# Kernel tuning notes

Hardware: AMD Instinct MI355X
Metric: run time of the kernel (lower is better)

The kernel has to match this reference:

```python
import jax, jax.numpy as jnp
import numpy as np

DIM = 256; SEQ = 2048; WIN = 64; HEADS = 4; RANK = 32; LAYERS = 3; VOCAB = 32000
EPS = 1e-6

def _unit(v):
    # unit_normalize_values: project onto unit sphere along feature dim
    return v / jnp.maximum(jnp.linalg.norm(v, axis=-1, keepdims=True), EPS)

def _signed_softmax(s):
    # signed_softmax_state: sign(s) * softmax(|s|) over nodes
    return jnp.sign(s) * jax.nn.softmax(jnp.abs(s), axis=-1)

def setup_inputs() -> dict:
    key = jax.random.key(0)
    ks = jax.random.split(key, 10)
    d = DIM
    return {
        "input_ids": jax.random.randint(ks[0], (2, SEQ), 0, VOCAB, dtype=jnp.int32),
        "emb": 0.02 * jax.random.normal(ks[1], (VOCAB, d), jnp.float32),
        "pos_emb": 0.02 * jax.random.normal(ks[2], (SEQ, d), jnp.float32),
        "anchor_val": 0.02 * jax.random.normal(ks[3], (d,), jnp.float32),
        "anchor_state": jnp.zeros((), jnp.float32),
        "Ws": 0.02 * jax.random.normal(ks[4], (d,), jnp.float32),
        "bs": jnp.zeros((), jnp.float32),
        "U": 0.02 * jax.random.normal(ks[5], (LAYERS, d, HEADS, RANK), jnp.float32),
        "V": 0.02 * jax.random.normal(ks[6], (LAYERS, d, HEADS, RANK), jnp.float32),
        "W1": 0.02 * jax.random.normal(ks[7], (LAYERS, d, 2 * d), jnp.float32),
        "b1": jnp.zeros((LAYERS, 2 * d), jnp.float32),
        "W2": 0.02 * jax.random.normal(ks[8], (LAYERS, 2 * d, d), jnp.float32),
        "b2": jnp.zeros((LAYERS, d), jnp.float32),
    }

def _forward(emb, pos_emb, anchor_val, anchor_state, Ws, bs, U, V, W1, b1, W2, b2, input_ids):
    B, S = input_ids.shape
    tok = emb[input_ids] + pos_emb[None, :S]          # [B,S,D]
    state_src = tok                                    # state projected from pre-unit-norm values
    tok = _unit(tok)
    tstate = state_src @ Ws + bs                       # [B,S] scalar state per node
    val = jnp.concatenate([jnp.broadcast_to(_unit(anchor_val), (B, 1, DIM)), tok], axis=1)
    state = jnp.concatenate([jnp.broadcast_to(anchor_state, (B, 1)), tstate], axis=1)
    N = S + 1
    offs = jnp.arange(-WIN, WIN + 1)
    idx = jnp.arange(N)[:, None] + offs[None, :]       # [N,K]
    valid = (idx >= 0) & (idx < N)
    idxc = jnp.clip(idx, 0, N - 1)
    inv_sqrt_r = np.float32(1.0 / np.sqrt(RANK))
    for l in range(LAYERS):
        q = jnp.einsum('bnd,dhr->bnhr', val, U[l])
        k = jnp.einsum('bnd,dhr->bnhr', val, V[l])
        knb = k[:, idxc]                               # [B,N,K,H,R] window gather
        s = jnp.einsum('bnhr,bnkhr->bnkh', q, knb) * inv_sqrt_r
        s = s.max(axis=-1)                             # max head-aggregate [B,N,K]
        a = jnp.where(valid, jnp.abs(s), -jnp.inf)
        wgt = jnp.where(valid, jnp.sign(s) * jax.nn.softmax(a, axis=-1), 0.0)  # signed-abs-softmax edges
        dval = jnp.einsum('bnk,bnkd->bnd', wgt, val[:, idxc])
        dstate = jnp.sum(wgt * state[:, idxc], axis=-1)
        # apply_delta: residual + norm(identity) + unit-norm + touched-mask where
        updated = val + dval
        nv = _unit(updated)
        touched = jnp.max(jnp.abs(jax.lax.stop_gradient(dval)), axis=-1, keepdims=True) > 0
        val = jnp.where(touched, nv, updated)
        state = _signed_softmax(state + dstate)
        # residual feed-forward then re-unit-norm
        h = jax.nn.gelu(jnp.einsum('bnd,dh->bnh', val, W1[l]) + b1[l], approximate=False)
        val = _unit(val + jnp.einsum('bnh,hd->bnd', h, W2[l]) + b2[l])
    return state, val

def reference(input_ids, emb, pos_emb, anchor_val, anchor_state, Ws, bs, U, V, W1, b1, W2, b2):
    return _forward(emb, pos_emb, anchor_val, anchor_state, Ws, bs, U, V, W1, b1, W2, b2, input_ids)
```

## Files before the change

### kernel.cpp

```cpp
#include <hip/hip_runtime.h>
#include <hip/hip_bf16.h>
#include <math.h>

#define BB 2
#define SS 2048
#define NN 2049
#define MM (BB*NN)
#define DD 256
#define HR 128
#define NHEAD 4
#define WINW 64
#define DFF 512
#define EPSF 1e-6f
#define TB8 257

typedef __attribute__((ext_vector_type(8))) short bf16x8;
typedef __attribute__((ext_vector_type(4))) float f32x4;

__device__ __forceinline__ float wave_sum(float v) {
    v += __shfl_down(v, 32, 64); v += __shfl_down(v, 16, 64);
    v += __shfl_down(v, 8, 64);  v += __shfl_down(v, 4, 64);
    v += __shfl_down(v, 2, 64);  v += __shfl_down(v, 1, 64);
    return v;
}
__device__ __forceinline__ float wave_max(float v) {
    v = fmaxf(v, __shfl_down(v, 32, 64)); v = fmaxf(v, __shfl_down(v, 16, 64));
    v = fmaxf(v, __shfl_down(v, 8, 64));  v = fmaxf(v, __shfl_down(v, 4, 64));
    v = fmaxf(v, __shfl_down(v, 2, 64));  v = fmaxf(v, __shfl_down(v, 1, 64));
    return v;
}
__device__ __forceinline__ float block_sum(float v, float* red) {
    v = wave_sum(v);
    __syncthreads();
    if ((threadIdx.x & 63) == 0) red[threadIdx.x >> 6] = v;
    __syncthreads();
    return red[0] + red[1] + red[2] + red[3];
}
__device__ __forceinline__ float sgnf(float x) {
    return (x > 0.f) ? 1.f : ((x < 0.f) ? -1.f : 0.f);
}
__device__ __forceinline__ ushort f2b(float x) {
    __hip_bfloat16 h = __float2bfloat16(x);
    return *(ushort*)&h;
}
__device__ __forceinline__ float b2f(ushort u) {
    unsigned int v = ((unsigned int)u) << 16;
    return *(float*)&v;
}
__device__ __forceinline__ void split3(float x, ushort& h, ushort& m, ushort& l) {
    h = f2b(x);
    float r1 = x - b2f(h);
    m = f2b(r1);
    l = f2b(r1 - b2f(m));
}
__device__ __forceinline__ void pack_map(int e, int N, int& k, int& n) {
    int j = e & 7;
    int l = (e >> 3) & 63;
    int c = e >> 9;
    int ntiles = N >> 4;
    int kt = c / ntiles, nt = c - kt * ntiles;
    k = kt * 32 + ((l >> 4) << 3) + j;
    n = nt * 16 + (l & 15);
}
__device__ __forceinline__ void dma16(const ushort* g, ushort* lds) {
    __builtin_amdgcn_global_load_lds(
        (const __attribute__((address_space(1))) unsigned int*)g,
        (__attribute__((address_space(3))) unsigned int*)lds,
        16, 0, 0);
}

__global__ void packall_kernel(const float* __restrict__ W1, const float* __restrict__ W2,
                               const float* __restrict__ U,  const float* __restrict__ V,
                               ushort* __restrict__ W1ph, ushort* __restrict__ W1pl,
                               ushort* __restrict__ W2ph, ushort* __restrict__ W2pl,
                               ushort* __restrict__ U0, ushort* __restrict__ U1,
                               ushort* __restrict__ U2,
                               ushort* __restrict__ V0, ushort* __restrict__ V1,
                               ushort* __restrict__ V2) {
    int idx = blockIdx.x * 256 + threadIdx.x;
    int l = idx / 327680;
    int r = idx - l * 327680;
    if (l >= 3) return;
    int k, n;
    if (r < 131072) {
        int e = r;
        pack_map(e, 512, k, n);
        float s = W1[(size_t)l * 131072 + (size_t)k * 512 + n];
        ushort h = f2b(s);
        W1ph[(size_t)l * 131072 + e] = h;
        W1pl[(size_t)l * 131072 + e] = f2b(s - b2f(h));
    } else if (r < 262144) {
        int e = r - 131072;
        pack_map(e, 256, k, n);
        float s = W2[(size_t)l * 131072 + (size_t)k * 256 + n];
        ushort h = f2b(s);
        W2ph[(size_t)l * 131072 + e] = h;
        W2pl[(size_t)l * 131072 + e] = f2b(s - b2f(h));
    } else if (r < 294912) {
        int e = r - 262144;
        pack_map(e, 128, k, n);
        ushort h, m, lo;
        split3(U[(size_t)l * 32768 + (size_t)k * 128 + n], h, m, lo);
        U0[(size_t)l * 32768 + e] = h;
        U1[(size_t)l * 32768 + e] = m;
        U2[(size_t)l * 32768 + e] = lo;
    } else {
        int e = r - 294912;
        pack_map(e, 128, k, n);
        ushort h, m, lo;
        split3(V[(size_t)l * 32768 + (size_t)k * 128 + n], h, m, lo);
        V0[(size_t)l * 32768 + e] = h;
        V1[(size_t)l * 32768 + e] = m;
        V2[(size_t)l * 32768 + e] = lo;
    }
}

__global__ void embed_kernel(const int* __restrict__ ids,
                             const float* __restrict__ emb,
                             const float* __restrict__ pos,
                             const float* __restrict__ anchor_val,
                             const float* __restrict__ anchor_state,
                             const float* __restrict__ Ws,
                             const float* __restrict__ bs,
                             float* __restrict__ val,
                             ushort* __restrict__ v0, ushort* __restrict__ v1,
                             ushort* __restrict__ v2,
                             float* __restrict__ state) {
    __shared__ float red[4];
    int row = blockIdx.x;
    int t = threadIdx.x;
    int b = row / NN, n = row % NN;
    float e;
    if (n == 0) {
        e = anchor_val[t];
    } else {
        int id = ids[b * SS + (n - 1)];
        e = emb[(size_t)id * DD + t] + pos[(size_t)(n - 1) * DD + t];
    }
    float ss = block_sum(e * e, red);
    float ts = block_sum(e * Ws[t], red);
    float rn = 1.f / fmaxf(sqrtf(ss), EPSF);
    float o = e * rn;
    size_t oi = (size_t)row * DD + t;
    val[oi] = o;
    ushort h, m, lo;
    split3(o, h, m, lo);
    v0[oi] = h; v1[oi] = m; v2[oi] = lo;
    if (t == 0) state[row] = (n == 0) ? anchor_state[0] : (ts + bs[0]);
}

__global__ __launch_bounds__(256, 2)
void proj_kernel(const ushort* __restrict__ X0, const ushort* __restrict__ X1,
                 const ushort* __restrict__ X2,
                 const ushort* __restrict__ U0, const ushort* __restrict__ U1,
                 const ushort* __restrict__ U2,
                 const ushort* __restrict__ V0, const ushort* __restrict__ V1,
                 const ushort* __restrict__ V2,
                 ushort* __restrict__ q0, ushort* __restrict__ q1,
                 ushort* __restrict__ q2,
                 ushort* __restrict__ k0, ushort* __restrict__ k1,
                 ushort* __restrict__ k2) {
    __shared__ __align__(16) ushort stage[2][24 * 512];
    int t = threadIdx.x;
    int w = t >> 6, l = t & 63;
    int lm = l & 15, quad = l >> 4;
    int m0 = blockIdx.x * 16;
    bool isQ = (blockIdx.y == 0);
    const ushort* P0 = isQ ? U0 : V0;
    const ushort* P1 = isQ ? U1 : V1;
    const ushort* P2 = isQ ? U2 : V2;
    const ushort* P[3] = {P0, P1, P2};
    int row0 = m0 + lm; if (row0 > MM - 1) row0 = MM - 1;

    #pragma unroll
    for (int i = 0; i < 6; i++) {
        int c = w * 6 + i;
        int p = c >> 3, ntl = c & 7;
        dma16(P[p] + ((size_t)(0 * 8 + ntl) * 64 + l) * 8,
              &stage[0][c * 512 + l * 8]);
    }
    __syncthreads();

    f32x4 acc[2];
    acc[0] = (f32x4)(0.f); acc[1] = (f32x4)(0.f);
    for (int kt = 0; kt < 8; kt++) {
        int cur = kt & 1;
        if (kt < 7) {
            #pragma unroll
            for (int i = 0; i < 6; i++) {
                int c = w * 6 + i;
                int p = c >> 3, ntl = c & 7;
                dma16(P[p] + ((size_t)((kt + 1) * 8 + ntl) * 64 + l) * 8,
                      &stage[cur ^ 1][c * 512 + l * 8]);
            }
        }
        int ko = kt * 32 + quad * 8;
        bf16x8 a0 = *(const bf16x8*)(X0 + (size_t)row0 * DD + ko);
        bf16x8 a1 = *(const bf16x8*)(X1 + (size_t)row0 * DD + ko);
        bf16x8 a2 = *(const bf16x8*)(X2 + (size_t)row0 * DD + ko);
        #pragma unroll
        for (int jj = 0; jj < 2; jj++) {
            int ntl = w * 2 + jj;
            bf16x8 b0 = *(const bf16x8*)&stage[cur][(0 * 8 + ntl) * 512 + l * 8];
            bf16x8 b1 = *(const bf16x8*)&stage[cur][(1 * 8 + ntl) * 512 + l * 8];
            bf16x8 b2 = *(const bf16x8*)&stage[cur][(2 * 8 + ntl) * 512 + l * 8];
            acc[jj] = __builtin_amdgcn_mfma_f32_16x16x32_bf16(a0, b0, acc[jj], 0, 0, 0);
            acc[jj] = __builtin_amdgcn_mfma_f32_16x16x32_bf16(a0, b1, acc[jj], 0, 0, 0);
            acc[jj] = __builtin_amdgcn_mfma_f32_16x16x32_bf16(a1, b0, acc[jj], 0, 0, 0);
            acc[jj] = __builtin_amdgcn_mfma_f32_16x16x32_bf16(a1, b1, acc[jj], 0, 0, 0);
            acc[jj] = __builtin_amdgcn_mfma_f32_16x16x32_bf16(a0, b2, acc[jj], 0, 0, 0);
            acc[jj] = __builtin_amdgcn_mfma_f32_16x16x32_bf16(a2, b0, acc[jj], 0, 0, 0);
        }
        __syncthreads();
    }
    ushort* o0 = isQ ? q0 : k0;
    ushort* o1 = isQ ? q1 : k1;
    ushort* o2 = isQ ? q2 : k2;
    #pragma unroll
    for (int jj = 0; jj < 2; jj++) {
        int n = (w * 2 + jj) * 16 + lm;
        #pragma unroll
        for (int r = 0; r < 4; r++) {
            int tok = m0 + quad * 4 + r;
            if (tok < MM) {
                ushort h, m, lo;
                split3(acc[jj][r], h, m, lo);
                size_t oi = (size_t)tok * HR + n;
                o0[oi] = h; o1[oi] = m; o2[oi] = lo;
            }
        }
    }
}

__global__ __launch_bounds__(256, 2)
void attn_kernel(const float* __restrict__ val_in,
                 const float* __restrict__ state_in,
                 const ushort* __restrict__ q0, const ushort* __restrict__ q1,
                 const ushort* __restrict__ q2,
                 const ushort* __restrict__ k0, const ushort* __restrict__ k1,
                 const ushort* __restrict__ k2,
                 float* __restrict__ val_out,
                 ushort* __restrict__ vbH, ushort* __restrict__ vbM,
                 float* __restrict__ dstate_out) {
    __shared__ float sc4[NHEAD][8][148];
    __shared__ float wgt2[144][12];
    __shared__ float redS[8][4];
    __shared__ float redM[8][4];

    int b = blockIdx.x / TB8;
    int n0 = (blockIdx.x % TB8) * 8;
    int t = threadIdx.x;
    int w = t >> 6, l = t & 63;
    int lm = l & 15, quad = l >> 4;

    {
        int qrow = n0 + (lm & 7);
        if (qrow > NN - 1) qrow = NN - 1;
        size_t qa = ((size_t)(b * NN + qrow)) * HR + w * 32 + quad * 8;
        bf16x8 a0 = *(const bf16x8*)(q0 + qa);
        bf16x8 a1 = *(const bf16x8*)(q1 + qa);
        bf16x8 a2 = *(const bf16x8*)(q2 + qa);
        bf16x8 kf0[9], kf1[9], kf2[9];
        #pragma unroll
        for (int jt = 0; jt < 9; jt++) {
            int j = n0 - 64 + jt * 16 + lm;
            j = (j < 0) ? 0 : ((j > NN - 1) ? NN - 1 : j);
            size_t ka = ((size_t)(b * NN + j)) * HR + w * 32 + quad * 8;
            kf0[jt] = *(const bf16x8*)(k0 + ka);
            kf1[jt] = *(const bf16x8*)(k1 + ka);
            kf2[jt] = *(const bf16x8*)(k2 + ka);
        }
        #pragma unroll
        for (int jt = 0; jt < 9; jt++) {
            f32x4 acc = (f32x4)(0.f);
            acc = __builtin_amdgcn_mfma_f32_16x16x32_bf16(a0, kf0[jt], acc, 0, 0, 0);
            acc = __builtin_amdgcn_mfma_f32_16x16x32_bf16(a0, kf1[jt], acc, 0, 0, 0);
            acc = __builtin_amdgcn_mfma_f32_16x16x32_bf16(a1, kf0[jt], acc, 0, 0, 0);
            acc = __builtin_amdgcn_mfma_f32_16x16x32_bf16(a1, kf1[jt], acc, 0, 0, 0);
            acc = __builtin_amdgcn_mfma_f32_16x16x32_bf16(a0, kf2[jt], acc, 0, 0, 0);
            acc = __builtin_amdgcn_mfma_f32_16x16x32_bf16(a2, kf0[jt], acc, 0, 0, 0);
            if (quad < 2) {
                #pragma unroll
                for (int r = 0; r < 4; r++)
                    sc4[w][quad * 4 + r][jt * 16 + lm] = acc[r];
            }
        }
    }
    __syncthreads();

    {
        int m = t >> 5, p = t & 31;
        int n = n0 + m;
        bool tokv = (n < NN);
        float sv[5]; bool vv[5];
        float mx = -INFINITY;
        #pragma unroll
        for (int i = 0; i < 5; i++) {
            int tap = p + 32 * i;
            bool inb = (tap < 144);
            int tapc = inb ? tap : 0;
            int j = n0 - 64 + tapc;
            float s0 = sc4[0][m][tapc], s1 = sc4[1][m][tapc];
            float s2 = sc4[2][m][tapc], s3 = sc4[3][m][tapc];
            float s = fmaxf(fmaxf(s0, s1), fmaxf(s2, s3)) * 0.17677669529663687f;
            bool v = inb && tokv && (tap >= m) && (tap <= m + 128) && (j >= 0) && (j < NN);
            sv[i] = s; vv[i] = v;
            if (v) mx = fmaxf(mx, fabsf(s));
        }
        for (int off = 16; off > 0; off >>= 1) mx = fmaxf(mx, __shfl_xor(mx, off, 64));
        float ee[5];
        float sum = 0.f;
        #pragma unroll
        for (int i = 0; i < 5; i++) {
            ee[i] = vv[i] ? expf(fabsf(sv[i]) - mx) : 0.f;
            sum += ee[i];
        }
        for (int off = 16; off > 0; off >>= 1) sum += __shfl_xor(sum, off, 64);
        float inv = (sum > 0.f) ? 1.f / sum : 0.f;
        float ds = 0.f;
        #pragma unroll
        for (int i = 0; i < 5; i++) {
            int tap = p + 32 * i;
            if (tap < 144) {
                float wg = vv[i] ? sgnf(sv[i]) * ee[i] * inv : 0.f;
                wgt2[tap][m] = wg;
                if (vv[i]) ds += wg * state_in[b * NN + (n0 - 64 + tap)];
            }
        }
        for (int off = 16; off > 0; off >>= 1) ds += __shfl_xor(ds, off, 64);
        if (p == 0 && tokv) dstate_out[b * NN + n] = ds;
    }
    __syncthreads();

    {
        int d = (t >> 2) * 4;
        int tg = t & 3;
        int tok0 = tg * 2, tok1 = tg * 2 + 1;
        int jlo = (n0 >= 64) ? 0 : (64 - n0);
        int jhi = NN - 1 - n0 + 64; if (jhi > 135) jhi = 135;
        const float* vbase = val_in + ((size_t)(b * NN + n0 - 64)) * DD + d;
        f32x4 acc0 = (f32x4)(0.f), acc1 = (f32x4)(0.f);
        int jj = jlo;
        for (; jj + 3 <= jhi; jj += 4) {
            f32x4 v0 = *(const f32x4*)(vbase + (size_t)(jj + 0) * DD);
            f32x4 v1 = *(const f32x4*)(vbase + (size_t)(jj + 1) * DD);
            f32x4 v2 = *(const f32x4*)(vbase + (size_t)(jj + 2) * DD);
            f32x4 v3 = *(const f32x4*)(vbase + (size_t)(jj + 3) * DD);
            float wa0 = wgt2[jj + 0][tok0], wa1 = wgt2[jj + 0][tok1];
            float wb0 = wgt2[jj + 1][tok0], wb1 = wgt2[jj + 1][tok1];
            float wc0 = wgt2[jj + 2][tok0], wc1 = wgt2[jj + 2][tok1];
            float wd0 = wgt2[jj + 3][tok0], wd1 = wgt2[jj + 3][tok1];
            #pragma unroll
            for (int c = 0; c < 4; c++) {
                acc0[c] += v0[c] * wa0 + v1[c] * wb0 + v2[c] * wc0 + v3[c] * wd0;
                acc1[c] += v0[c] * wa1 + v1[c] * wb1 + v2[c] * wc1 + v3[c] * wd1;
            }
        }
        for (; jj <= jhi; jj++) {
            f32x4 v = *(const f32x4*)(vbase + (size_t)jj * DD);
            float w0 = wgt2[jj][tok0], w1 = wgt2[jj][tok1];
            #pragma unroll
            for (int c = 0; c < 4; c++) {
                acc0[c] += v[c] * w0;
                acc1[c] += v[c] * w1;
            }
        }
        f32x4 u[2]; f32x4 ac[2]; ac[0] = acc0; ac[1] = acc1;
        #pragma unroll
        for (int ti = 0; ti < 2; ti++) {
            int tok = tg * 2 + ti;
            int n = n0 + tok;
            f32x4 vold = (f32x4)(0.f);
            if (n < NN) vold = *(const f32x4*)(val_in + ((size_t)(b * NN + n)) * DD + d);
            u[ti] = vold + ac[ti];
            float s = u[ti][0]*u[ti][0] + u[ti][1]*u[ti][1] + u[ti][2]*u[ti][2] + u[ti][3]*u[ti][3];
            float mb = fmaxf(fmaxf(fabsf(ac[ti][0]), fabsf(ac[ti][1])),
                             fmaxf(fabsf(ac[ti][2]), fabsf(ac[ti][3])));
            for (int off = 4; off <= 32; off <<= 1) {
                s += __shfl_xor(s, off, 64);
                mb = fmaxf(mb, __shfl_xor(mb, off, 64));
            }
            if ((l >> 2) == 0) { redS[tok][w] = s; redM[tok][w] = mb; }
        }
        __syncthreads();
        #pragma unroll
        for (int ti = 0; ti < 2; ti++) {
            int tok = tg * 2 + ti;
            int n = n0 + tok;
            if (n < NN) {
                float ss = redS[tok][0] + redS[tok][1] + redS[tok][2] + redS[tok][3];
                float mab = fmaxf(fmaxf(redM[tok][0], redM[tok][1]),
                                  fmaxf(redM[tok][2], redM[tok][3]));
                float rn = 1.f / fmaxf(sqrtf(ss), EPSF);
                f32x4 o = u[ti];
                if (mab > 0.f) { o[0] *= rn; o[1] *= rn; o[2] *= rn; o[3] *= rn; }
                size_t oi = ((size_t)(b * NN + n)) * DD + d;
                *(f32x4*)(val_out + oi) = o;
                ushort4 hv, mv;
                {
                    ushort h0 = f2b(o[0]); hv.x = h0; mv.x = f2b(o[0] - b2f(h0));
                    ushort h1 = f2b(o[1]); hv.y = h1; mv.y = f2b(o[1] - b2f(h1));
                    ushort h2 = f2b(o[2]); hv.z = h2; mv.z = f2b(o[2] - b2f(h2));
                    ushort h3 = f2b(o[3]); hv.w = h3; mv.w = f2b(o[3] - b2f(h3));
                }
                *(ushort4*)(vbH + oi) = hv;
                *(ushort4*)(vbM + oi) = mv;
            }
        }
    }
}

__global__ __launch_bounds__(256, 2)
void ffn1_kernel(const ushort* __restrict__ XbH, const ushort* __restrict__ XbM,
                 const ushort* __restrict__ W1h, const ushort* __restrict__ W1l,
                 const float*  __restrict__ b1,
                 ushort* __restrict__ Hh, ushort* __restrict__ Hl,
                 const float* __restrict__ state_in, const float* __restrict__ dstate,
                 float* __restrict__ state_out) {
    __shared__ __align__(16) ushort stage[2][32 * 512];
    int t = threadIdx.x;

    if (blockIdx.x == 257) {
        float* red = (float*)&stage[0][0];
        int b = blockIdx.y;
        float lmax = -INFINITY;
        for (int n = t; n < NN; n += 256) {
            float x = state_in[b * NN + n] + dstate[b * NN + n];
            lmax = fmaxf(lmax, fabsf(x));
        }
        lmax = wave_max(lmax);
        if ((t & 63) == 0) red[t >> 6] = lmax;
        __syncthreads();
        float m = fmaxf(fmaxf(red[0], red[1]), fmaxf(red[2], red[3]));
        float lsum = 0.f;
        for (int n = t; n < NN; n += 256)
            lsum += expf(fabsf(state_in[b * NN + n] + dstate[b * NN + n]) - m);
        lsum = wave_sum(lsum);
        __syncthreads();
        if ((t & 63) == 0) red[4 + (t >> 6)] = lsum;
        __syncthreads();
        float inv = 1.f / (red[4] + red[5] + red[6] + red[7]);
        for (int n = t; n < NN; n += 256) {
            float x = state_in[b * NN + n] + dstate[b * NN + n];
            state_out[b * NN + n] = sgnf(x) * expf(fabsf(x) - m) * inv;
        }
        return;
    }

    int w = t >> 6, l = t & 63;
    int lm = l & 15, quad = l >> 4;
    int m0 = blockIdx.x * 16;
    int nh = blockIdx.y;
    int row0 = m0 + lm; if (row0 > MM - 1) row0 = MM - 1;

    #pragma unroll
    for (int i = 0; i < 8; i++) {
        int c = w * 8 + i;
        int p = c >> 4, ntl = c & 15;
        const ushort* src = (p ? W1l : W1h) + ((size_t)(0 * 32 + nh * 16 + ntl) * 64 + l) * 8;
        dma16(src, &stage[0][c * 512 + l * 8]);
    }
    __syncthreads();

    f32x4 acc[4];
    #pragma unroll
    for (int jj = 0; jj < 4; jj++) acc[jj] = (f32x4)(0.f);

    for (int kt = 0; kt < 8; kt++) {
        int cur = kt & 1;
        if (kt < 7) {
            #pragma unroll
            for (int i = 0; i < 8; i++) {
                int c = w * 8 + i;
                int p = c >> 4, ntl = c & 15;
                const ushort* src = (p ? W1l : W1h) +
                    ((size_t)((kt + 1) * 32 + nh * 16 + ntl) * 64 + l) * 8;
                dma16(src, &stage[cur ^ 1][c * 512 + l * 8]);
            }
        }
        int ko = kt * 32 + quad * 8;
        bf16x8 ah = *(const bf16x8*)(XbH + (size_t)row0 * DD + ko);
        bf16x8 am = *(const bf16x8*)(XbM + (size_t)row0 * DD + ko);
        #pragma unroll
        for (int jj = 0; jj < 4; jj++) {
            int ntl = w * 4 + jj;
            bf16x8 bh = *(const bf16x8*)&stage[cur][ntl * 512 + l * 8];
            bf16x8 bl = *(const bf16x8*)&stage[cur][(16 + ntl) * 512 + l * 8];
            acc[jj] = __builtin_amdgcn_mfma_f32_16x16x32_bf16(ah, bh, acc[jj], 0, 0, 0);
            acc[jj] = __builtin_amdgcn_mfma_f32_16x16x32_bf16(am, bh, acc[jj], 0, 0, 0);
            acc[jj] = __builtin_amdgcn_mfma_f32_16x16x32_bf16(ah, bl, acc[jj], 0, 0, 0);
        }
        __syncthreads();
    }
    #pragma unroll
    for (int jj = 0; jj < 4; jj++) {
        int gn = nh * 256 + (w * 4 + jj) * 16 + lm;
        float bb = b1[gn];
        #pragma unroll
        for (int r = 0; r < 4; r++) {
            int tok = m0 + quad * 4 + r;
            if (tok < MM) {
                float x = acc[jj][r] + bb;
                float g = 0.5f * x * (1.f + erff(x * 0.70710678118654752f));
                ushort gh = f2b(g);
                size_t oi = (size_t)tok * DFF + gn;
                Hh[oi] = gh;
                Hl[oi] = f2b(g - b2f(gh));
            }
        }
    }
}

__global__ __launch_bounds__(256, 2)
void ffn2_kernel(const ushort* __restrict__ Hh, const ushort* __restrict__ Hl,
                 const float*  __restrict__ Xf,
                 const ushort* __restrict__ W2h, const ushort* __restrict__ W2l,
                 const float*  __restrict__ b2,
                 float* __restrict__ Yb) {
    __shared__ __align__(16) ushort stage[2][16 * 512];
    int t = threadIdx.x;
    int w = t >> 6, l = t & 63;
    int lm = l & 15, quad = l >> 4;
    int m0 = blockIdx.x * 16;
    int nh = blockIdx.y;
    int row0 = m0 + lm; if (row0 > MM - 1) row0 = MM - 1;

    #pragma unroll
    for (int i = 0; i < 4; i++) {
        int c = w * 4 + i;
        int p = c >> 3, ntl = c & 7;
        const ushort* src = (p ? W2l : W2h) + ((size_t)(0 * 16 + nh * 8 + ntl) * 64 + l) * 8;
        dma16(src, &stage[0][c * 512 + l * 8]);
    }
    __syncthreads();

    f32x4 acc[2];
    acc[0] = (f32x4)(0.f); acc[1] = (f32x4)(0.f);

    for (int kt = 0; kt < 16; kt++) {
        int cur = kt & 1;
        if (kt < 15) {
            #pragma unroll
            for (int i = 0; i < 4; i++) {
                int c = w * 4 + i;
                int p = c >> 3, ntl = c & 7;
                const ushort* src = (p ? W2l : W2h) +
                    ((size_t)((kt + 1) * 16 + nh * 8 + ntl) * 64 + l) * 8;
                dma16(src, &stage[cur ^ 1][c * 512 + l * 8]);
            }
        }
        int ko = kt * 32 + quad * 8;
        bf16x8 ah = *(const bf16x8*)(Hh + (size_t)row0 * DFF + ko);
        bf16x8 al = *(const bf16x8*)(Hl + (size_t)row0 * DFF + ko);
        #pragma unroll
        for (int jj = 0; jj < 2; jj++) {
            int ntl = w * 2 + jj;
            bf16x8 bh = *(const bf16x8*)&stage[cur][ntl * 512 + l * 8];
            bf16x8 bl = *(const bf16x8*)&stage[cur][(8 + ntl) * 512 + l * 8];
            acc[jj] = __builtin_amdgcn_mfma_f32_16x16x32_bf16(ah, bh, acc[jj], 0, 0, 0);
            acc[jj] = __builtin_amdgcn_mfma_f32_16x16x32_bf16(al, bh, acc[jj], 0, 0, 0);
            acc[jj] = __builtin_amdgcn_mfma_f32_16x16x32_bf16(ah, bl, acc[jj], 0, 0, 0);
        }
        __syncthreads();
    }
    #pragma unroll
    for (int jj = 0; jj < 2; jj++) {
        int gn = nh * 128 + (w * 2 + jj) * 16 + lm;
        float bb = b2[gn];
        #pragma unroll
        for (int r = 0; r < 4; r++) {
            int tok = m0 + quad * 4 + r;
            if (tok < MM) {
                size_t oi = (size_t)tok * DD + gn;
                Yb[oi] = Xf[oi] + acc[jj][r] + bb;
            }
        }
    }
}

__global__ void ffn3_kernel(const float* __restrict__ Yb,
                            float* __restrict__ val_out,
                            ushort* __restrict__ o0, ushort* __restrict__ o1,
                            ushort* __restrict__ o2) {
    int t = threadIdx.x;
    int w = t >> 6, l = t & 63;
    int row = blockIdx.x * 4 + w;
    if (row >= MM) return;
    f32x4 y = *(const f32x4*)(Yb + (size_t)row * DD + l * 4);
    float s = y[0]*y[0] + y[1]*y[1] + y[2]*y[2] + y[3]*y[3];
    #pragma unroll
    for (int off = 1; off < 64; off <<= 1) s += __shfl_xor(s, off, 64);
    float rn = 1.f / fmaxf(sqrtf(s), EPSF);
    f32x4 o;
    o[0] = y[0] * rn; o[1] = y[1] * rn; o[2] = y[2] * rn; o[3] = y[3] * rn;
    size_t oi = (size_t)row * DD + l * 4;
    *(f32x4*)(val_out + oi) = o;
    ushort4 h4, m4, l4;
    ushort hh, mm, ll;
    split3(o[0], hh, mm, ll); h4.x = hh; m4.x = mm; l4.x = ll;
    split3(o[1], hh, mm, ll); h4.y = hh; m4.y = mm; l4.y = ll;
    split3(o[2], hh, mm, ll); h4.z = hh; m4.z = mm; l4.z = ll;
    split3(o[3], hh, mm, ll); h4.w = hh; m4.w = mm; l4.w = ll;
    *(ushort4*)(o0 + oi) = h4;
    *(ushort4*)(o1 + oi) = m4;
    *(ushort4*)(o2 + oi) = l4;
}

extern "C" void kernel_launch(void* const* d_in, const int* in_sizes, int n_in,
                              void* d_out, int out_size, void* d_ws, size_t ws_size,
                              hipStream_t stream) {
    const int*   ids          = (const int*)d_in[0];
    const float* emb          = (const float*)d_in[1];
    const float* pos          = (const float*)d_in[2];
    const float* anchor_val   = (const float*)d_in[3];
    const float* anchor_state = (const float*)d_in[4];
    const float* Ws           = (const float*)d_in[5];
    const float* bs           = (const float*)d_in[6];
    const float* U            = (const float*)d_in[7];
    const float* V            = (const float*)d_in[8];
    const float* W1           = (const float*)d_in[9];
    const float* b1           = (const float*)d_in[10];
    const float* W2           = (const float*)d_in[11];
    const float* b2           = (const float*)d_in[12];
    float* out = (float*)d_out;

    ushort* p = (ushort*)d_ws;
    ushort* vA0 = p; p += (size_t)MM * DD;
    ushort* vA1 = p; p += (size_t)MM * DD;
    ushort* vA2 = p; p += (size_t)MM * DD;
    ushort* vB0 = p; p += (size_t)MM * DD;
    ushort* vB1 = p; p += (size_t)MM * DD;
    ushort* q0b = p; p += (size_t)MM * HR;
    ushort* q1b = p; p += (size_t)MM * HR;
    ushort* q2b = p; p += (size_t)MM * HR;
    ushort* k0b = p; p += (size_t)MM * HR;
    ushort* k1b = p; p += (size_t)MM * HR;
    ushort* k2b = p; p += (size_t)MM * HR;
    ushort* Hh  = p; p += (size_t)MM * DFF;
    ushort* Hl  = p; p += (size_t)MM * DFF;
    ushort* W1ph = p; p += 3 * 131072;
    ushort* W1pl = p; p += 3 * 131072;
    ushort* W2ph = p; p += 3 * 131072;
    ushort* W2pl = p; p += 3 * 131072;
    ushort* U0p = p; p += 3 * 32768;
    ushort* U1p = p; p += 3 * 32768;
    ushort* U2p = p; p += 3 * 32768;
    ushort* V0p = p; p += 3 * 32768;
    ushort* V1p = p; p += 3 * 32768;
    ushort* V2p = p; p += 3 * 32768;
    float* f = (float*)p;
    float* valA = f; f += (size_t)MM * DD;
    float* valB = f; f += (size_t)MM * DD;
    float* st0  = f; f += MM;
    float* st1  = f; f += MM;
    float* dst  = f; f += MM;
    float* Yb   = valA;

    packall_kernel<<<3840, 256, 0, stream>>>(W1, W2, U, V,
                                             W1ph, W1pl, W2ph, W2pl,
                                             U0p, U1p, U2p, V0p, V1p, V2p);

    embed_kernel<<<MM, 256, 0, stream>>>(ids, emb, pos, anchor_val, anchor_state,
                                         Ws, bs, valA, vA0, vA1, vA2, st0);
    float* s_in = st0;
    float* s_out = st1;
    for (int l = 0; l < 3; l++) {
        proj_kernel<<<dim3(257, 2), 256, 0, stream>>>(
            vA0, vA1, vA2,
            U0p + (size_t)l * 32768, U1p + (size_t)l * 32768, U2p + (size_t)l * 32768,
            V0p + (size_t)l * 32768, V1p + (size_t)l * 32768, V2p + (size_t)l * 32768,
            q0b, q1b, q2b, k0b, k1b, k2b);
        attn_kernel<<<BB * TB8, 256, 0, stream>>>(valA, s_in,
                                                  q0b, q1b, q2b, k0b, k1b, k2b,
                                                  valB, vB0, vB1, dst);
        ffn1_kernel<<<dim3(258, 2), 256, 0, stream>>>(
            vB0, vB1,
            W1ph + (size_t)l * 131072, W1pl + (size_t)l * 131072, b1 + (size_t)l * DFF,
            Hh, Hl,
            s_in, dst, (l == 2) ? out : s_out);
        ffn2_kernel<<<dim3(257, 2), 256, 0, stream>>>(
            Hh, Hl, valB,
            W2ph + (size_t)l * 131072, W2pl + (size_t)l * 131072, b2 + (size_t)l * DD,
            Yb);
        ffn3_kernel<<<(MM + 3) / 4, 256, 0, stream>>>(
            Yb, (l == 2) ? (out + MM) : valA, vA0, vA1, vA2);
        float* tmp = s_in; s_in = s_out; s_out = tmp;
    }
}
```

Measured before the change: 358.0 us.

## Fuse FFN up-proj, GELU, down-proj, residual and unit-norm into one kernel

Replaces the three FFN kernels (ffn1, ffn2, ffn3) with a single kernel. Each 16-row block loads its fp32 value rows into LDS and splits them to bf16 hi/mid in registers. It computes both halves of the hidden layer into LDS, runs the down-projection, then adds the residual and unit-normalises before writing the outputs. This removes the global round-trips for the hidden activations, the bf16 value copies from attention and the Yb buffer, plus two launches per layer. In exchange the grid drops from about 514 blocks to 258 with one block per CU. The kernel also uses much more LDS, which may reduce parallelism and latency hiding.

```diff
diff --git a/kernel.cpp b/kernel.cpp
--- a/kernel.cpp
+++ b/kernel.cpp
@@ -240,7 +240,6 @@
                  const ushort* __restrict__ k0, const ushort* __restrict__ k1,
                  const ushort* __restrict__ k2,
                  float* __restrict__ val_out,
-                 ushort* __restrict__ vbH, ushort* __restrict__ vbM,
                  float* __restrict__ dstate_out) {
     __shared__ float sc4[NHEAD][8][148];
     __shared__ float wgt2[144][12];
@@ -396,53 +395,56 @@
                 if (mab > 0.f) { o[0] *= rn; o[1] *= rn; o[2] *= rn; o[3] *= rn; }
                 size_t oi = ((size_t)(b * NN + n)) * DD + d;
                 *(f32x4*)(val_out + oi) = o;
-                ushort4 hv, mv;
-                {
-                    ushort h0 = f2b(o[0]); hv.x = h0; mv.x = f2b(o[0] - b2f(h0));
-                    ushort h1 = f2b(o[1]); hv.y = h1; mv.y = f2b(o[1] - b2f(h1));
-                    ushort h2 = f2b(o[2]); hv.z = h2; mv.z = f2b(o[2] - b2f(h2));
-                    ushort h3 = f2b(o[3]); hv.w = h3; mv.w = f2b(o[3] - b2f(h3));
-                }
-                *(ushort4*)(vbH + oi) = hv;
-                *(ushort4*)(vbM + oi) = mv;
-            }
-        }
-    }
-}
-
-__global__ __launch_bounds__(256, 2)
-void ffn1_kernel(const ushort* __restrict__ XbH, const ushort* __restrict__ XbM,
-                 const ushort* __restrict__ W1h, const ushort* __restrict__ W1l,
-                 const float*  __restrict__ b1,
-                 ushort* __restrict__ Hh, ushort* __restrict__ Hl,
-                 const float* __restrict__ state_in, const float* __restrict__ dstate,
-                 float* __restrict__ state_out) {
+            }
+        }
+    }
+}
+
+__global__ __launch_bounds__(256, 1)
+void ffn_fused(const float* __restrict__ Xf,
+               const ushort* __restrict__ W1h, const ushort* __restrict__ W1l,
+               const float*  __restrict__ b1,
+               const ushort* __restrict__ W2h, const ushort* __restrict__ W2l,
+               const float*  __restrict__ b2,
+               float* __restrict__ val_out,
+               ushort* __restrict__ o0, ushort* __restrict__ o1,
+               ushort* __restrict__ o2,
+               const float* __restrict__ state_in, const float* __restrict__ dstate,
+               float* __restrict__ state_out) {
     __shared__ __align__(16) ushort stage[2][32 * 512];
+    __shared__ __align__(16) ushort HtH[16 * 520];
+    __shared__ __align__(16) ushort HtL[16 * 520];
+    __shared__ float lv[16 * 260];
+    __shared__ float red[16][17];
+    __shared__ float rrn[16];
+
     int t = threadIdx.x;
 
     if (blockIdx.x == 257) {
-        float* red = (float*)&stage[0][0];
-        int b = blockIdx.y;
-        float lmax = -INFINITY;
-        for (int n = t; n < NN; n += 256) {
-            float x = state_in[b * NN + n] + dstate[b * NN + n];
-            lmax = fmaxf(lmax, fabsf(x));
-        }
-        lmax = wave_max(lmax);
-        if ((t & 63) == 0) red[t >> 6] = lmax;
-        __syncthreads();
-        float m = fmaxf(fmaxf(red[0], red[1]), fmaxf(red[2], red[3]));
-        float lsum = 0.f;
-        for (int n = t; n < NN; n += 256)
-            lsum += expf(fabsf(state_in[b * NN + n] + dstate[b * NN + n]) - m);
-        lsum = wave_sum(lsum);
-        __syncthreads();
-        if ((t & 63) == 0) red[4 + (t >> 6)] = lsum;
-        __syncthreads();
-        float inv = 1.f / (red[4] + red[5] + red[6] + red[7]);
-        for (int n = t; n < NN; n += 256) {
-            float x = state_in[b * NN + n] + dstate[b * NN + n];
-            state_out[b * NN + n] = sgnf(x) * expf(fabsf(x) - m) * inv;
+        float* rd = (float*)HtH;
+        for (int b = 0; b < 2; b++) {
+            float lmax = -INFINITY;
+            for (int n = t; n < NN; n += 256) {
+                float x = state_in[b * NN + n] + dstate[b * NN + n];
+                lmax = fmaxf(lmax, fabsf(x));
+            }
+            lmax = wave_max(lmax);
+            if ((t & 63) == 0) rd[t >> 6] = lmax;
+            __syncthreads();
+            float m = fmaxf(fmaxf(rd[0], rd[1]), fmaxf(rd[2], rd[3]));
+            float lsum = 0.f;
+            for (int n = t; n < NN; n += 256)
+                lsum += expf(fabsf(state_in[b * NN + n] + dstate[b * NN + n]) - m);
+            lsum = wave_sum(lsum);
+            __syncthreads();
+            if ((t & 63) == 0) rd[4 + (t >> 6)] = lsum;
+            __syncthreads();
+            float inv = 1.f / (rd[4] + rd[5] + rd[6] + rd[7]);
+            for (int n = t; n < NN; n += 256) {
+                float x = state_in[b * NN + n] + dstate[b * NN + n];
+                state_out[b * NN + n] = sgnf(x) * expf(fabsf(x) - m) * inv;
+            }
+            __syncthreads();
         }
         return;
     }
@@ -450,160 +452,168 @@
     int w = t >> 6, l = t & 63;
     int lm = l & 15, quad = l >> 4;
     int m0 = blockIdx.x * 16;
-    int nh = blockIdx.y;
-    int row0 = m0 + lm; if (row0 > MM - 1) row0 = MM - 1;
+
+    {
+        int row = t >> 4, c0 = (t & 15) * 16;
+        int gr = m0 + row; if (gr > MM - 1) gr = MM - 1;
+        const float* src = Xf + (size_t)gr * DD + c0;
+        f32x4 v0 = *(const f32x4*)(src + 0);
+        f32x4 v1 = *(const f32x4*)(src + 4);
+        f32x4 v2 = *(const f32x4*)(src + 8);
+        f32x4 v3 = *(const f32x4*)(src + 12);
+        *(f32x4*)&lv[row * 260 + c0 + 0]  = v0;
+        *(f32x4*)&lv[row * 260 + c0 + 4]  = v1;
+        *(f32x4*)&lv[row * 260 + c0 + 8]  = v2;
+        *(f32x4*)&lv[row * 260 + c0 + 12] = v3;
+    }
+    __syncthreads();
+
+    bf16x8 afh[8], afm[8];
+    #pragma unroll
+    for (int kt = 0; kt < 8; kt++) {
+        int ko = kt * 32 + quad * 8;
+        f32x4 x0 = *(const f32x4*)&lv[lm * 260 + ko];
+        f32x4 x1 = *(const f32x4*)&lv[lm * 260 + ko + 4];
+        bf16x8 h, m;
+        #pragma unroll
+        for (int j = 0; j < 4; j++) {
+            ushort hh = f2b(x0[j]); h[j] = (short)hh; m[j] = (short)f2b(x0[j] - b2f(hh));
+        }
+        #pragma unroll
+        for (int j = 0; j < 4; j++) {
+            ushort hh = f2b(x1[j]); h[4+j] = (short)hh; m[4+j] = (short)f2b(x1[j] - b2f(hh));
+        }
+        afh[kt] = h; afm[kt] = m;
+    }
+
+    for (int nh = 0; nh < 2; nh++) {
+        __syncthreads();
+        #pragma unroll
+        for (int i = 0; i < 8; i++) {
+            int c = w * 8 + i;
+            int p = c >> 4, ntl = c & 15;
+            const ushort* src = (p ? W1l : W1h) +
+                ((size_t)(0 * 32 + nh * 16 + ntl) * 64 + l) * 8;
+            dma16(src, &stage[0][c * 512 + l * 8]);
+        }
+        __syncthreads();
+        f32x4 acc[4];
+        #pragma unroll
+        for (int jj = 0; jj < 4; jj++) acc[jj] = (f32x4)(0.f);
+        for (int kt = 0; kt < 8; kt++) {
+            int cur = kt & 1;
+            if (kt < 7) {
+                #pragma unroll
+                for (int i = 0; i < 8; i++) {
+                    int c = w * 8 + i;
+                    int p = c >> 4, ntl = c & 15;
+                    const ushort* src = (p ? W1l : W1h) +
+                        ((size_t)((kt + 1) * 32 + nh * 16 + ntl) * 64 + l) * 8;
+                    dma16(src, &stage[cur ^ 1][c * 512 + l * 8]);
+                }
+            }
+            #pragma unroll
+            for (int jj = 0; jj < 4; jj++) {
+                int ntl = w * 4 + jj;
+                bf16x8 bh = *(const bf16x8*)&stage[cur][ntl * 512 + l * 8];
+                bf16x8 bl = *(const bf16x8*)&stage[cur][(16 + ntl) * 512 + l * 8];
+                acc[jj] = __builtin_amdgcn_mfma_f32_16x16x32_bf16(afh[kt], bh, acc[jj], 0, 0, 0);
+                acc[jj] = __builtin_amdgcn_mfma_f32_16x16x32_bf16(afm[kt], bh, acc[jj], 0, 0, 0);
+                acc[jj] = __builtin_amdgcn_mfma_f32_16x16x32_bf16(afh[kt], bl, acc[jj], 0, 0, 0);
+            }
+            __syncthreads();
+        }
+        #pragma unroll
+        for (int jj = 0; jj < 4; jj++) {
+            int gn = nh * 256 + (w * 4 + jj) * 16 + lm;
+            float bb = b1[gn];
+            #pragma unroll
+            for (int r = 0; r < 4; r++) {
+                float x = acc[jj][r] + bb;
+                float g = 0.5f * x * (1.f + erff(x * 0.70710678118654752f));
+                ushort gh = f2b(g);
+                HtH[(quad * 4 + r) * 520 + gn] = gh;
+                HtL[(quad * 4 + r) * 520 + gn] = f2b(g - b2f(gh));
+            }
+        }
+    }
+    __syncthreads();
 
     #pragma unroll
     for (int i = 0; i < 8; i++) {
         int c = w * 8 + i;
         int p = c >> 4, ntl = c & 15;
-        const ushort* src = (p ? W1l : W1h) + ((size_t)(0 * 32 + nh * 16 + ntl) * 64 + l) * 8;
+        const ushort* src = (p ? W2l : W2h) + ((size_t)(0 * 16 + ntl) * 64 + l) * 8;
         dma16(src, &stage[0][c * 512 + l * 8]);
     }
     __syncthreads();
-
-    f32x4 acc[4];
+    f32x4 acc2[4];
     #pragma unroll
-    for (int jj = 0; jj < 4; jj++) acc[jj] = (f32x4)(0.f);
-
-    for (int kt = 0; kt < 8; kt++) {
+    for (int jj = 0; jj < 4; jj++) acc2[jj] = (f32x4)(0.f);
+    for (int kt = 0; kt < 16; kt++) {
         int cur = kt & 1;
-        if (kt < 7) {
+        if (kt < 15) {
             #pragma unroll
             for (int i = 0; i < 8; i++) {
                 int c = w * 8 + i;
                 int p = c >> 4, ntl = c & 15;
-                const ushort* src = (p ? W1l : W1h) +
-                    ((size_t)((kt + 1) * 32 + nh * 16 + ntl) * 64 + l) * 8;
+                const ushort* src = (p ? W2l : W2h) +
+                    ((size_t)((kt + 1) * 16 + ntl) * 64 + l) * 8;
                 dma16(src, &stage[cur ^ 1][c * 512 + l * 8]);
             }
         }
-        int ko = kt * 32 + quad * 8;
-        bf16x8 ah = *(const bf16x8*)(XbH + (size_t)row0 * DD + ko);
-        bf16x8 am = *(const bf16x8*)(XbM + (size_t)row0 * DD + ko);
+        bf16x8 ah2 = *(const bf16x8*)(HtH + lm * 520 + kt * 32 + quad * 8);
+        bf16x8 al2 = *(const bf16x8*)(HtL + lm * 520 + kt * 32 + quad * 8);
         #pragma unroll
         for (int jj = 0; jj < 4; jj++) {
             int ntl = w * 4 + jj;
             bf16x8 bh = *(const bf16x8*)&stage[cur][ntl * 512 + l * 8];
             bf16x8 bl = *(const bf16x8*)&stage[cur][(16 + ntl) * 512 + l * 8];
-            acc[jj] = __builtin_amdgcn_mfma_f32_16x16x32_bf16(ah, bh, acc[jj], 0, 0, 0);
-            acc[jj] = __builtin_amdgcn_mfma_f32_16x16x32_bf16(am, bh, acc[jj], 0, 0, 0);
-            acc[jj] = __builtin_amdgcn_mfma_f32_16x16x32_bf16(ah, bl, acc[jj], 0, 0, 0);
+            acc2[jj] = __builtin_amdgcn_mfma_f32_16x16x32_bf16(ah2, bh, acc2[jj], 0, 0, 0);
+            acc2[jj] = __builtin_amdgcn_mfma_f32_16x16x32_bf16(al2, bh, acc2[jj], 0, 0, 0);
+            acc2[jj] = __builtin_amdgcn_mfma_f32_16x16x32_bf16(ah2, bl, acc2[jj], 0, 0, 0);
         }
         __syncthreads();
     }
+
     #pragma unroll
     for (int jj = 0; jj < 4; jj++) {
-        int gn = nh * 256 + (w * 4 + jj) * 16 + lm;
-        float bb = b1[gn];
+        int gn = (w * 4 + jj) * 16 + lm;
+        float bb = b2[gn];
         #pragma unroll
         for (int r = 0; r < 4; r++) {
-            int tok = m0 + quad * 4 + r;
-            if (tok < MM) {
-                float x = acc[jj][r] + bb;
-                float g = 0.5f * x * (1.f + erff(x * 0.70710678118654752f));
-                ushort gh = f2b(g);
-                size_t oi = (size_t)tok * DFF + gn;
-                Hh[oi] = gh;
-                Hl[oi] = f2b(g - b2f(gh));
-            }
-        }
-    }
-}
-
-__global__ __launch_bounds__(256, 2)
-void ffn2_kernel(const ushort* __restrict__ Hh, const ushort* __restrict__ Hl,
-                 const float*  __restrict__ Xf,
-                 const ushort* __restrict__ W2h, const ushort* __restrict__ W2l,
-                 const float*  __restrict__ b2,
-                 float* __restrict__ Yb) {
-    __shared__ __align__(16) ushort stage[2][16 * 512];
-    int t = threadIdx.x;
-    int w = t >> 6, l = t & 63;
-    int lm = l & 15, quad = l >> 4;
-    int m0 = blockIdx.x * 16;
-    int nh = blockIdx.y;
-    int row0 = m0 + lm; if (row0 > MM - 1) row0 = MM - 1;
-
+            int row = quad * 4 + r;
+            lv[row * 260 + gn] += acc2[jj][r] + bb;
+        }
+    }
+    __syncthreads();
+    {
+        int row = t >> 4, p2 = t & 15;
+        float s = 0.f;
+        #pragma unroll
+        for (int i = 0; i < 16; i++) { float y = lv[row * 260 + p2 * 16 + i]; s += y * y; }
+        red[row][p2] = s;
+    }
+    __syncthreads();
+    if (t < 16) {
+        float s = 0.f;
+        #pragma unroll
+        for (int i = 0; i < 16; i++) s += red[t][i];
+        rrn[t] = 1.f / fmaxf(sqrtf(s), EPSF);
+    }
+    __syncthreads();
     #pragma unroll
-    for (int i = 0; i < 4; i++) {
-        int c = w * 4 + i;
-        int p = c >> 3, ntl = c & 7;
-        const ushort* src = (p ? W2l : W2h) + ((size_t)(0 * 16 + nh * 8 + ntl) * 64 + l) * 8;
-        dma16(src, &stage[0][c * 512 + l * 8]);
-    }
-    __syncthreads();
-
-    f32x4 acc[2];
-    acc[0] = (f32x4)(0.f); acc[1] = (f32x4)(0.f);
-
-    for (int kt = 0; kt < 16; kt++) {
-        int cur = kt & 1;
-        if (kt < 15) {
-            #pragma unroll
-            for (int i = 0; i < 4; i++) {
-                int c = w * 4 + i;
-                int p = c >> 3, ntl = c & 7;
-                const ushort* src = (p ? W2l : W2h) +
-                    ((size_t)((kt + 1) * 16 + nh * 8 + ntl) * 64 + l) * 8;
-                dma16(src, &stage[cur ^ 1][c * 512 + l * 8]);
-            }
-        }
-        int ko = kt * 32 + quad * 8;
-        bf16x8 ah = *(const bf16x8*)(Hh + (size_t)row0 * DFF + ko);
-        bf16x8 al = *(const bf16x8*)(Hl + (size_t)row0 * DFF + ko);
-        #pragma unroll
-        for (int jj = 0; jj < 2; jj++) {
-            int ntl = w * 2 + jj;
-            bf16x8 bh = *(const bf16x8*)&stage[cur][ntl * 512 + l * 8];
-            bf16x8 bl = *(const bf16x8*)&stage[cur][(8 + ntl) * 512 + l * 8];
-            acc[jj] = __builtin_amdgcn_mfma_f32_16x16x32_bf16(ah, bh, acc[jj], 0, 0, 0);
-            acc[jj] = __builtin_amdgcn_mfma_f32_16x16x32_bf16(al, bh, acc[jj], 0, 0, 0);
-            acc[jj] = __builtin_amdgcn_mfma_f32_16x16x32_bf16(ah, bl, acc[jj], 0, 0, 0);
-        }
-        __syncthreads();
-    }
-    #pragma unroll
-    for (int jj = 0; jj < 2; jj++) {
-        int gn = nh * 128 + (w * 2 + jj) * 16 + lm;
-        float bb = b2[gn];
-        #pragma unroll
-        for (int r = 0; r < 4; r++) {
-            int tok = m0 + quad * 4 + r;
-            if (tok < MM) {
-                size_t oi = (size_t)tok * DD + gn;
-                Yb[oi] = Xf[oi] + acc[jj][r] + bb;
-            }
-        }
-    }
-}
-
-__global__ void ffn3_kernel(const float* __restrict__ Yb,
-                            float* __restrict__ val_out,
-                            ushort* __restrict__ o0, ushort* __restrict__ o1,
-                            ushort* __restrict__ o2) {
-    int t = threadIdx.x;
-    int w = t >> 6, l = t & 63;
-    int row = blockIdx.x * 4 + w;
-    if (row >= MM) return;
-    f32x4 y = *(const f32x4*)(Yb + (size_t)row * DD + l * 4);
-    float s = y[0]*y[0] + y[1]*y[1] + y[2]*y[2] + y[3]*y[3];
-    #pragma unroll
-    for (int off = 1; off < 64; off <<= 1) s += __shfl_xor(s, off, 64);
-    float rn = 1.f / fmaxf(sqrtf(s), EPSF);
-    f32x4 o;
-    o[0] = y[0] * rn; o[1] = y[1] * rn; o[2] = y[2] * rn; o[3] = y[3] * rn;
-    size_t oi = (size_t)row * DD + l * 4;
-    *(f32x4*)(val_out + oi) = o;
-    ushort4 h4, m4, l4;
-    ushort hh, mm, ll;
-    split3(o[0], hh, mm, ll); h4.x = hh; m4.x = mm; l4.x = ll;
-    split3(o[1], hh, mm, ll); h4.y = hh; m4.y = mm; l4.y = ll;
-    split3(o[2], hh, mm, ll); h4.z = hh; m4.z = mm; l4.z = ll;
-    split3(o[3], hh, mm, ll); h4.w = hh; m4.w = mm; l4.w = ll;
-    *(ushort4*)(o0 + oi) = h4;
-    *(ushort4*)(o1 + oi) = m4;
-    *(ushort4*)(o2 + oi) = l4;
+    for (int m = 0; m < 16; m++) {
+        int row = m0 + m;
+        if (row < MM) {
+            float o = lv[m * 260 + t] * rrn[m];
+            size_t oi = (size_t)row * DD + t;
+            val_out[oi] = o;
+            ushort h, mm, lo;
+            split3(o, h, mm, lo);
+            o0[oi] = h; o1[oi] = mm; o2[oi] = lo;
+        }
+    }
 }
 
 extern "C" void kernel_launch(void* const* d_in, const int* in_sizes, int n_in,
@@ -628,16 +638,12 @@
     ushort* vA0 = p; p += (size_t)MM * DD;
     ushort* vA1 = p; p += (size_t)MM * DD;
     ushort* vA2 = p; p += (size_t)MM * DD;
-    ushort* vB0 = p; p += (size_t)MM * DD;
-    ushort* vB1 = p; p += (size_t)MM * DD;
     ushort* q0b = p; p += (size_t)MM * HR;
     ushort* q1b = p; p += (size_t)MM * HR;
     ushort* q2b = p; p += (size_t)MM * HR;
     ushort* k0b = p; p += (size_t)MM * HR;
     ushort* k1b = p; p += (size_t)MM * HR;
     ushort* k2b = p; p += (size_t)MM * HR;
-    ushort* Hh  = p; p += (size_t)MM * DFF;
-    ushort* Hl  = p; p += (size_t)MM * DFF;
     ushort* W1ph = p; p += 3 * 131072;
     ushort* W1pl = p; p += 3 * 131072;
     ushort* W2ph = p; p += 3 * 131072;
@@ -654,7 +660,6 @@
     float* st0  = f; f += MM;
     float* st1  = f; f += MM;
     float* dst  = f; f += MM;
-    float* Yb   = valA;
 
     packall_kernel<<<3840, 256, 0, stream>>>(W1, W2, U, V,
                                              W1ph, W1pl, W2ph, W2pl,
@@ -672,18 +677,13 @@
             q0b, q1b, q2b, k0b, k1b, k2b);
         attn_kernel<<<BB * TB8, 256, 0, stream>>>(valA, s_in,
                                                   q0b, q1b, q2b, k0b, k1b, k2b,
-                                                  valB, vB0, vB1, dst);
-        ffn1_kernel<<<dim3(258, 2), 256, 0, stream>>>(
-            vB0, vB1,
+                                                  valB, dst);
+        ffn_fused<<<258, 256, 0, stream>>>(
+            valB,
             W1ph + (size_t)l * 131072, W1pl + (size_t)l * 131072, b1 + (size_t)l * DFF,
-            Hh, Hl,
+            W2ph + (size_t)l * 131072, W2pl + (size_t)l * 131072, b2 + (size_t)l * DD,
+            (l == 2) ? (out + MM) : valA, vA0, vA1, vA2,
             s_in, dst, (l == 2) ? out : s_out);
-        ffn2_kernel<<<dim3(257, 2), 256, 0, stream>>>(
-            Hh, Hl, valB,
-            W2ph + (size_t)l * 131072, W2pl + (size_t)l * 131072, b2 + (size_t)l * DD,
-            Yb);
-        ffn3_kernel<<<(MM + 3) / 4, 256, 0, stream>>>(
-            Yb, (l == 2) ? (out + MM) : valA, vA0, vA1, vA2);
         float* tmp = s_in; s_in = s_out; s_out = tmp;
     }
 }
```

Result: slower. 382.2 us (+6.7%).

## Fuse FFN2 GEMM with residual unit-normalization and bf16 split epilogue

Applied to the files above, without the earlier changes.

The second FFN GEMM now computes all 256 output columns per block, where it previously split them across two blocks along grid.y. That lets it run the row L2 normalization and the 3-way bf16 split in the epilogue through a small shared-memory reduction, so the separate ffn3 kernel and the Yb round-trip through global memory go away. In exchange the grid is halved to 257 blocks, each doing twice the MFMA work with twice the LDS staging, which lowers parallelism. The output stores are also now scalar and strided rather than vectorized.

```diff
diff --git a/kernel.cpp b/kernel.cpp
--- a/kernel.cpp
+++ b/kernel.cpp
@@ -512,40 +512,43 @@
 }
 
 __global__ __launch_bounds__(256, 2)
-void ffn2_kernel(const ushort* __restrict__ Hh, const ushort* __restrict__ Hl,
-                 const float*  __restrict__ Xf,
-                 const ushort* __restrict__ W2h, const ushort* __restrict__ W2l,
-                 const float*  __restrict__ b2,
-                 float* __restrict__ Yb) {
-    __shared__ __align__(16) ushort stage[2][16 * 512];
+void ffn2_full(const ushort* __restrict__ Hh, const ushort* __restrict__ Hl,
+               const float*  __restrict__ Xf,
+               const ushort* __restrict__ W2h, const ushort* __restrict__ W2l,
+               const float*  __restrict__ b2,
+               float* __restrict__ val_out,
+               ushort* __restrict__ o0, ushort* __restrict__ o1,
+               ushort* __restrict__ o2) {
+    __shared__ __align__(16) ushort stage[2][32 * 512];
+    __shared__ float red[16][5];
     int t = threadIdx.x;
     int w = t >> 6, l = t & 63;
     int lm = l & 15, quad = l >> 4;
     int m0 = blockIdx.x * 16;
-    int nh = blockIdx.y;
     int row0 = m0 + lm; if (row0 > MM - 1) row0 = MM - 1;
 
     #pragma unroll
-    for (int i = 0; i < 4; i++) {
-        int c = w * 4 + i;
-        int p = c >> 3, ntl = c & 7;
-        const ushort* src = (p ? W2l : W2h) + ((size_t)(0 * 16 + nh * 8 + ntl) * 64 + l) * 8;
+    for (int i = 0; i < 8; i++) {
+        int c = w * 8 + i;
+        int p = c >> 4, ntl = c & 15;
+        const ushort* src = (p ? W2l : W2h) + ((size_t)(0 * 16 + ntl) * 64 + l) * 8;
         dma16(src, &stage[0][c * 512 + l * 8]);
     }
     __syncthreads();
 
-    f32x4 acc[2];
-    acc[0] = (f32x4)(0.f); acc[1] = (f32x4)(0.f);
+    f32x4 acc2[4];
+    #pragma unroll
+    for (int jj = 0; jj < 4; jj++) acc2[jj] = (f32x4)(0.f);
 
     for (int kt = 0; kt < 16; kt++) {
         int cur = kt & 1;
         if (kt < 15) {
             #pragma unroll
-            for (int i = 0; i < 4; i++) {
-                int c = w * 4 + i;
-                int p = c >> 3, ntl = c & 7;
+            for (int i = 0; i < 8; i++) {
+                int c = w * 8 + i;
+                int p = c >> 4, ntl = c & 15;
                 const ushort* src = (p ? W2l : W2h) +
-                    ((size_t)((kt + 1) * 16 + nh * 8 + ntl) * 64 + l) * 8;
+                    ((size_t)((kt + 1) * 16 + ntl) * 64 + l) * 8;
                 dma16(src, &stage[cur ^ 1][c * 512 + l * 8]);
             }
         }
@@ -553,57 +556,63 @@
         bf16x8 ah = *(const bf16x8*)(Hh + (size_t)row0 * DFF + ko);
         bf16x8 al = *(const bf16x8*)(Hl + (size_t)row0 * DFF + ko);
         #pragma unroll
-        for (int jj = 0; jj < 2; jj++) {
-            int ntl = w * 2 + jj;
+        for (int jj = 0; jj < 4; jj++) {
+            int ntl = w * 4 + jj;
             bf16x8 bh = *(const bf16x8*)&stage[cur][ntl * 512 + l * 8];
-            bf16x8 bl = *(const bf16x8*)&stage[cur][(8 + ntl) * 512 + l * 8];
-            acc[jj] = __builtin_amdgcn_mfma_f32_16x16x32_bf16(ah, bh, acc[jj], 0, 0, 0);
-            acc[jj] = __builtin_amdgcn_mfma_f32_16x16x32_bf16(al, bh, acc[jj], 0, 0, 0);
-            acc[jj] = __builtin_amdgcn_mfma_f32_16x16x32_bf16(ah, bl, acc[jj], 0, 0, 0);
+            bf16x8 bl = *(const bf16x8*)&stage[cur][(16 + ntl) * 512 + l * 8];
+            acc2[jj] = __builtin_amdgcn_mfma_f32_16x16x32_bf16(ah, bh, acc2[jj], 0, 0, 0);
+            acc2[jj] = __builtin_amdgcn_mfma_f32_16x16x32_bf16(al, bh, acc2[jj], 0, 0, 0);
+            acc2[jj] = __builtin_amdgcn_mfma_f32_16x16x32_bf16(ah, bl, acc2[jj], 0, 0, 0);
         }
         __syncthreads();
     }
-    #pragma unroll
-    for (int jj = 0; jj < 2; jj++) {
-        int gn = nh * 128 + (w * 2 + jj) * 16 + lm;
+
+    float yv[4][4];
+    #pragma unroll
+    for (int jj = 0; jj < 4; jj++) {
+        int gn = (w * 4 + jj) * 16 + lm;
         float bb = b2[gn];
+        #pragma unroll
+        for (int r = 0; r < 4; r++) {
+            int tok = m0 + quad * 4 + r;
+            int tokc = (tok > MM - 1) ? (MM - 1) : tok;
+            yv[jj][r] = Xf[(size_t)tokc * DD + gn] + acc2[jj][r] + bb;
+        }
+    }
+    #pragma unroll
+    for (int r = 0; r < 4; r++) {
+        float s = yv[0][r]*yv[0][r] + yv[1][r]*yv[1][r]
+                + yv[2][r]*yv[2][r] + yv[3][r]*yv[3][r];
+        s += __shfl_xor(s, 1, 64);
+        s += __shfl_xor(s, 2, 64);
+        s += __shfl_xor(s, 4, 64);
+        s += __shfl_xor(s, 8, 64);
+        if (lm == 0) red[quad * 4 + r][w] = s;
+    }
+    __syncthreads();
+    float rnv[4];
+    #pragma unroll
+    for (int r = 0; r < 4; r++) {
+        int row = quad * 4 + r;
+        float ss = red[row][0] + red[row][1] + red[row][2] + red[row][3];
+        rnv[r] = 1.f / fmaxf(sqrtf(ss), EPSF);
+    }
+    #pragma unroll
+    for (int jj = 0; jj < 4; jj++) {
+        int gn = (w * 4 + jj) * 16 + lm;
         #pragma unroll
         for (int r = 0; r < 4; r++) {
             int tok = m0 + quad * 4 + r;
             if (tok < MM) {
+                float o = yv[jj][r] * rnv[r];
                 size_t oi = (size_t)tok * DD + gn;
-                Yb[oi] = Xf[oi] + acc[jj][r] + bb;
-            }
-        }
-    }
-}
-
-__global__ void ffn3_kernel(const float* __restrict__ Yb,
-                            float* __restrict__ val_out,
-                            ushort* __restrict__ o0, ushort* __restrict__ o1,
-                            ushort* __restrict__ o2) {
-    int t = threadIdx.x;
-    int w = t >> 6, l = t & 63;
-    int row = blockIdx.x * 4 + w;
-    if (row >= MM) return;
-    f32x4 y = *(const f32x4*)(Yb + (size_t)row * DD + l * 4);
-    float s = y[0]*y[0] + y[1]*y[1] + y[2]*y[2] + y[3]*y[3];
-    #pragma unroll
-    for (int off = 1; off < 64; off <<= 1) s += __shfl_xor(s, off, 64);
-    float rn = 1.f / fmaxf(sqrtf(s), EPSF);
-    f32x4 o;
-    o[0] = y[0] * rn; o[1] = y[1] * rn; o[2] = y[2] * rn; o[3] = y[3] * rn;
-    size_t oi = (size_t)row * DD + l * 4;
-    *(f32x4*)(val_out + oi) = o;
-    ushort4 h4, m4, l4;
-    ushort hh, mm, ll;
-    split3(o[0], hh, mm, ll); h4.x = hh; m4.x = mm; l4.x = ll;
-    split3(o[1], hh, mm, ll); h4.y = hh; m4.y = mm; l4.y = ll;
-    split3(o[2], hh, mm, ll); h4.z = hh; m4.z = mm; l4.z = ll;
-    split3(o[3], hh, mm, ll); h4.w = hh; m4.w = mm; l4.w = ll;
-    *(ushort4*)(o0 + oi) = h4;
-    *(ushort4*)(o1 + oi) = m4;
-    *(ushort4*)(o2 + oi) = l4;
+                val_out[oi] = o;
+                ushort h, mm, lo;
+                split3(o, h, mm, lo);
+                o0[oi] = h; o1[oi] = mm; o2[oi] = lo;
+            }
+        }
+    }
 }
 
 extern "C" void kernel_launch(void* const* d_in, const int* in_sizes, int n_in,
@@ -654,7 +663,6 @@
     float* st0  = f; f += MM;
     float* st1  = f; f += MM;
     float* dst  = f; f += MM;
-    float* Yb   = valA;
 
     packall_kernel<<<3840, 256, 0, stream>>>(W1, W2, U, V,
                                              W1ph, W1pl, W2ph, W2pl,
@@ -678,12 +686,10 @@
             W1ph + (size_t)l * 131072, W1pl + (size_t)l * 131072, b1 + (size_t)l * DFF,
             Hh, Hl,
             s_in, dst, (l == 2) ? out : s_out);
-        ffn2_kernel<<<dim3(257, 2), 256, 0, stream>>>(
+        ffn2_full<<<257, 256, 0, stream>>>(
             Hh, Hl, valB,
             W2ph + (size_t)l * 131072, W2pl + (size_t)l * 131072, b2 + (size_t)l * DD,
-            Yb);
-        ffn3_kernel<<<(MM + 3) / 4, 256, 0, stream>>>(
-            Yb, (l == 2) ? (out + MM) : valA, vA0, vA1, vA2);
+            (l == 2) ? (out + MM) : valA, vA0, vA1, vA2);
         float* tmp = s_in; s_in = s_out; s_out = tmp;
     }
 }
```

Result: no change. 359.3 us (+0.4%).
